# Kernel optimization log

Measured on AMD Instinct MI355X. Metric: run time of the kernel, lower is better.

Reference implementation:

```python
import jax, jax.numpy as jnp
import numpy as np
import math

B_SZ, L_SEQ, IN_DIM, D_MODEL, OUT_DIM = 8, 4096, 256, 512, 256
RMIN, RMAX = 0.8, 0.99


def setup_inputs() -> dict:
    key = jax.random.key(0)
    ks = jax.random.split(key, 9)
    inputs = jax.random.normal(ks[0], (B_SZ, L_SEQ, IN_DIM), dtype=jnp.float32)
    # A-parameterization per LRUBlock.init_A
    u1 = jax.random.uniform(ks[1], (D_MODEL,), dtype=jnp.float32)
    u2 = jax.random.uniform(ks[2], (D_MODEL,), dtype=jnp.float32)
    nu_log = jnp.log(-0.5 * jnp.log(u1 * (RMAX + RMIN) * (RMAX - RMIN) + RMIN ** 2))
    theta_log = jnp.log(2 * math.pi * u2)
    # NB: original stores gamma (not log gamma) and exponentiates it in forward; replicate.
    gamma_log = jnp.sqrt(1.0 - jnp.exp(-jnp.exp(nu_log)) ** 2)
    B_re = jax.random.uniform(ks[3], (D_MODEL, IN_DIM), dtype=jnp.float32) / math.sqrt(2 * IN_DIM)
    B_im = jax.random.uniform(ks[4], (D_MODEL, IN_DIM), dtype=jnp.float32) / math.sqrt(2 * IN_DIM)
    C_re = jax.random.uniform(ks[5], (OUT_DIM, D_MODEL), dtype=jnp.float32) / math.sqrt(D_MODEL)
    C_im = jax.random.uniform(ks[6], (OUT_DIM, D_MODEL), dtype=jnp.float32) / math.sqrt(D_MODEL)
    D = jax.random.uniform(ks[7], (OUT_DIM, IN_DIM), dtype=jnp.float32) / math.sqrt(IN_DIM)
    return {"inputs": inputs, "nu_log": nu_log, "theta_log": theta_log,
            "gamma_log": gamma_log, "B_re": B_re, "B_im": B_im,
            "C_re": C_re, "C_im": C_im, "D": D}


def reference(inputs, nu_log, theta_log, gamma_log, B_re, B_im, C_re, C_im, D):
    # skip connection: [b, l, in] x [out, in] -> [b, l, out]
    skip = jnp.einsum('blh,dh->bld', inputs, D)
    L = inputs.shape[1]
    # diagonal complex transition A = exp(-exp(nu) + i*exp(theta)), [d_model]
    A = jnp.exp(jax.lax.complex(-jnp.exp(nu_log), jnp.exp(theta_log)))
    Bc = jax.lax.complex(B_re, B_im) * jnp.exp(gamma_log)[:, None]
    # input projection u = inputs @ B^T : [b, l, d_model] complex64
    u = jnp.einsum('blh,dh->bld', inputs.astype(jnp.complex64), Bc)
    # convolution kernel H[d, t] = A[d]^t, linear conv via length-2L FFT
    H = A[:, None] ** jnp.arange(L)  # [d_model, L]
    n = 2 * L
    h_f = jnp.fft.fft(H, n=n, axis=1)          # [d_model, 2L]
    u_f = jnp.fft.fft(u, n=n, axis=1)          # [b, 2L, d_model]
    x = jnp.fft.ifft(u_f * h_f.T, axis=1)[:, :L]  # [b, L, d_model] complex64
    y = jnp.einsum('blh,nh->bln', x, jax.lax.complex(C_re, C_im)).real + skip
    return (x, y)
```

## Files before the change

kernel.cpp:

```cpp
#include <hip/hip_runtime.h>
#include <hip/hip_bf16.h>
#include <math.h>

#define B_SZ 8
#define L_SEQ 4096
#define IN_DIM 256
#define D_MODEL 512
#define OUT_DIM 256
#define M_ROWS (B_SZ*L_SEQ)
#define CH 64
#define NCH (L_SEQ/CH)

#define Y_OFF ((size_t)M_ROWS*D_MODEL)

#define XIM_B   ((size_t)0)
#define INPB_B  ((size_t)33554432)
#define WT_B    ((size_t)50331648)
#define CDT_B   ((size_t)50855936)
#define S_B     ((size_t)51511296)

typedef __attribute__((ext_vector_type(8))) short short8;
typedef __attribute__((ext_vector_type(4))) float f32x4;
typedef unsigned short ushort_t;
typedef unsigned int u32;

__device__ __forceinline__ unsigned short f2b(float f) {
    unsigned u = __float_as_uint(f);
    unsigned r = u + 0x7FFF + ((u >> 16) & 1);
    return (unsigned short)(r >> 16);
}
__device__ __forceinline__ float b2f(unsigned v) {
    return __uint_as_float(v << 16);
}
__device__ __forceinline__ unsigned pk2(float lo, float hi) {
    __hip_bfloat162 h = __float22bfloat162_rn(make_float2(lo, hi));
    return *(unsigned*)&h;
}
__device__ __forceinline__ void async16(const void* g, void* l) {
    __builtin_amdgcn_global_load_lds((const __attribute__((address_space(1))) u32*)g,
                                     (__attribute__((address_space(3))) u32*)l, 16, 0, 0);
}

__global__ __launch_bounds__(256) void cvt_inp(const float* __restrict__ inp, ushort_t* __restrict__ inpb) {
    size_t i = ((size_t)blockIdx.x*256 + threadIdx.x)*8;
    float4 a = *(const float4*)(inp + i);
    float4 b = *(const float4*)(inp + i + 4);
    unsigned v[4] = { pk2(a.x,a.y), pk2(a.z,a.w), pk2(b.x,b.y), pk2(b.z,b.w) };
    *(uint4*)(inpb + i) = *(uint4*)v;
}

__global__ void build_wt(const float* __restrict__ B_re, const float* __restrict__ B_im,
                         const float* __restrict__ gamma_log, ushort_t* __restrict__ Wt) {
    int idx = blockIdx.x*256 + threadIdx.x;
    int r = idx >> 8, h = idx & 255;
    int d = r >> 1, comp = r & 1;
    float eg = expf(gamma_log[d]);
    float v = (comp ? B_im[d*256 + h] : B_re[d*256 + h]) * eg;
    Wt[idx] = f2b(v);
}

__global__ void build_cdt(const float* __restrict__ C_re, const float* __restrict__ C_im,
                          const float* __restrict__ Dm, ushort_t* __restrict__ CDt) {
    int idx = blockIdx.x*256 + threadIdx.x;
    int n = idx / 1280, k = idx % 1280;
    float v;
    if      (k < 512)  v =  C_re[n*512 + k];
    else if (k < 1024) v = -C_im[n*512 + (k-512)];
    else               v =  Dm[n*256 + (k-1024)];
    CDt[idx] = f2b(v);
}

__global__ __launch_bounds__(256) void gemm_u(const ushort_t* __restrict__ inpb, const ushort_t* __restrict__ Wt,
                                              ushort_t* __restrict__ xpair) {
    __shared__ ushort_t Al[128*64];
    __shared__ ushort_t Bl[128*64];
    const int tid = threadIdx.x;
    int orig = blockIdx.x;
    int wg = (orig & 7) * 256 + (orig >> 3);
    const int row0 = (wg >> 3) * 128, col0 = (wg & 7) * 128;
    const int wave = tid >> 6, lane = tid & 63;
    const int wr = wave >> 1, wc = wave & 1;
    const int fr = lane & 15, kg = lane >> 4;
    const int grow = tid >> 3, ggr = tid & 7;
    f32x4 acc[4][4] = {};
    for (int k0 = 0; k0 < IN_DIM; k0 += 64) {
        __syncthreads();
        #pragma unroll
        for (int i = 0; i < 4; ++i) {
            int row = grow + i*32;
            async16(inpb + (size_t)(row0+row)*IN_DIM + k0 + ggr*8, &Al[(row*8 + ggr)*8]);
        }
        #pragma unroll
        for (int i = 0; i < 4; ++i) {
            int row = grow + i*32;
            async16(Wt + (size_t)(col0+row)*IN_DIM + k0 + ggr*8, &Bl[(row*8 + ggr)*8]);
        }
        __syncthreads();
        #pragma unroll
        for (int kk = 0; kk < 2; ++kk) {
            short8 af[4], bf[4];
            #pragma unroll
            for (int m = 0; m < 4; ++m) af[m] = *(const short8*)&Al[(wr*64 + m*16 + fr)*64 + kk*32 + kg*8];
            #pragma unroll
            for (int n = 0; n < 4; ++n) bf[n] = *(const short8*)&Bl[(wc*64 + n*16 + fr)*64 + kk*32 + kg*8];
            #pragma unroll
            for (int m = 0; m < 4; ++m)
                #pragma unroll
                for (int n = 0; n < 4; ++n)
                    acc[m][n] = __builtin_amdgcn_mfma_f32_16x16x32_bf16(af[m], bf[n], acc[m][n], 0, 0, 0);
        }
    }
    #pragma unroll
    for (int m = 0; m < 4; ++m)
        #pragma unroll
        for (int n = 0; n < 4; ++n) {
            int col = col0 + wc*64 + n*16 + fr;
            #pragma unroll
            for (int j = 0; j < 4; ++j) {
                int row = row0 + wr*64 + m*16 + kg*4 + j;
                xpair[(size_t)row*1024 + col] = f2b(acc[m][n][j]);
            }
        }
}

__global__ __launch_bounds__(256) void gemm_y(const float* __restrict__ xre, const ushort_t* __restrict__ xim,
                                              const ushort_t* __restrict__ inpb, const ushort_t* __restrict__ CDt,
                                              float* __restrict__ y) {
    __shared__ ushort_t Al[128*64];
    __shared__ ushort_t Bl[128*64];
    const int tid = threadIdx.x;
    int orig = blockIdx.x;
    int wg = (orig & 7) * 64 + (orig >> 3);
    const int row0 = (wg >> 1) * 128, col0 = (wg & 1) * 128;
    const int wave = tid >> 6, lane = tid & 63;
    const int wr = wave >> 1, wc = wave & 1;
    const int fr = lane & 15, kg = lane >> 4;
    const int grow = tid >> 3, ggr = tid & 7;
    const int crow = tid >> 1, csh = (tid & 1)*32;
    f32x4 acc[4][4] = {};
    for (int ks = 0; ks < 20; ++ks) {
        const int k0 = ks*64;
        __syncthreads();
        if (ks < 8) {
            const float* ap = xre + (size_t)(row0+crow)*D_MODEL + k0 + csh;
            unsigned v[16];
            #pragma unroll
            for (int i = 0; i < 8; ++i) {
                float4 f = *(const float4*)(ap + i*4);
                v[2*i]   = pk2(f.x, f.y);
                v[2*i+1] = pk2(f.z, f.w);
            }
            #pragma unroll
            for (int i = 0; i < 4; ++i) {
                int row = grow + i*32;
                async16(CDt + (size_t)(col0+row)*1280 + k0 + ggr*8, &Bl[(row*8 + ggr)*8]);
            }
            ushort_t* dst = &Al[crow*64 + csh];
            #pragma unroll
            for (int i = 0; i < 4; ++i) *(uint4*)(dst + i*8) = *(uint4*)&v[i*4];
        } else {
            const ushort_t* asrc;
            size_t stride; int kc;
            if (ks < 16) { asrc = xim;  stride = D_MODEL; kc = k0 - 512; }
            else         { asrc = inpb; stride = IN_DIM;  kc = k0 - 1024; }
            #pragma unroll
            for (int i = 0; i < 4; ++i) {
                int row = grow + i*32;
                async16(asrc + (size_t)(row0+row)*stride + kc + ggr*8, &Al[(row*8 + ggr)*8]);
            }
            #pragma unroll
            for (int i = 0; i < 4; ++i) {
                int row = grow + i*32;
                async16(CDt + (size_t)(col0+row)*1280 + k0 + ggr*8, &Bl[(row*8 + ggr)*8]);
            }
        }
        __syncthreads();
        #pragma unroll
        for (int kk = 0; kk < 2; ++kk) {
            short8 af[4], bf[4];
            #pragma unroll
            for (int m = 0; m < 4; ++m) af[m] = *(const short8*)&Al[(wr*64 + m*16 + fr)*64 + kk*32 + kg*8];
            #pragma unroll
            for (int n = 0; n < 4; ++n) bf[n] = *(const short8*)&Bl[(wc*64 + n*16 + fr)*64 + kk*32 + kg*8];
            #pragma unroll
            for (int m = 0; m < 4; ++m)
                #pragma unroll
                for (int n = 0; n < 4; ++n)
                    acc[m][n] = __builtin_amdgcn_mfma_f32_16x16x32_bf16(af[m], bf[n], acc[m][n], 0, 0, 0);
        }
    }
    #pragma unroll
    for (int m = 0; m < 4; ++m)
        #pragma unroll
        for (int n = 0; n < 4; ++n) {
            int col = col0 + wc*64 + n*16 + fr;
            #pragma unroll
            for (int j = 0; j < 4; ++j) {
                int row = row0 + wr*64 + m*16 + kg*4 + j;
                y[(size_t)row*OUT_DIM + col] = acc[m][n][j];
            }
        }
}

__global__ void scan_phase1(const unsigned* __restrict__ xp,
                            const float* __restrict__ nu_log, const float* __restrict__ theta_log,
                            float2* __restrict__ s) {
    int idx = blockIdx.x*256 + threadIdx.x;
    int d = idx & (D_MODEL-1);
    int c = (idx >> 9) & (NCH-1);
    int b = idx >> 15;
    float en = expf(nu_log[d]), et = expf(theta_log[d]);
    float mag = expf(-en);
    float ar = mag*cosf(et), ai = mag*sinf(et);
    float hr = 0.f, hi = 0.f;
    size_t off = ((size_t)(b*L_SEQ) + c*CH)*D_MODEL + d;
    #pragma unroll 4
    for (int j = 0; j < CH; ++j) {
        unsigned p = xp[off];
        float ur = b2f(p & 0xffffu), ui = b2f(p >> 16);
        float nr = ar*hr - ai*hi + ur;
        float ni = ar*hi + ai*hr + ui;
        hr = nr; hi = ni;
        off += D_MODEL;
    }
    s[idx] = make_float2(hr, hi);
}

__global__ void scan_phase2(const float* __restrict__ nu_log, const float* __restrict__ theta_log,
                            float2* __restrict__ s) {
    int idx = blockIdx.x*256 + threadIdx.x;
    int d = idx & (D_MODEL-1);
    int b = idx >> 9;
    float en = expf(nu_log[d]), et = expf(theta_log[d]);
    float mag = expf(-(float)CH*en);
    float ang = (float)CH*et;
    float aCr = mag*cosf(ang), aCi = mag*sinf(ang);
    float er = 0.f, ei = 0.f;
    float2* sp = s + (size_t)b*NCH*D_MODEL + d;
    for (int c8 = 0; c8 < NCH; c8 += 8) {
        float2 v[8];
        #pragma unroll
        for (int i = 0; i < 8; ++i) v[i] = sp[(size_t)(c8+i)*D_MODEL];
        #pragma unroll
        for (int i = 0; i < 8; ++i) {
            sp[(size_t)(c8+i)*D_MODEL] = make_float2(er, ei);
            float nr = aCr*er - aCi*ei + v[i].x;
            float ni = aCr*ei + aCi*er + v[i].y;
            er = nr; ei = ni;
        }
    }
}

__global__ void scan_phase3(unsigned* __restrict__ xp, ushort_t* __restrict__ xim,
                            const float* __restrict__ nu_log, const float* __restrict__ theta_log,
                            const float2* __restrict__ s) {
    int idx = blockIdx.x*256 + threadIdx.x;
    int d = idx & (D_MODEL-1);
    int c = (idx >> 9) & (NCH-1);
    int b = idx >> 15;
    float en = expf(nu_log[d]), et = expf(theta_log[d]);
    float mag = expf(-en);
    float ar = mag*cosf(et), ai = mag*sinf(et);
    float2 carry = s[idx];
    float hr = carry.x, hi = carry.y;
    size_t off = ((size_t)(b*L_SEQ) + c*CH)*D_MODEL + d;
    #pragma unroll 4
    for (int j = 0; j < CH; ++j) {
        unsigned p = xp[off];
        float ur = b2f(p & 0xffffu), ui = b2f(p >> 16);
        float nr = ar*hr - ai*hi + ur;
        float ni = ar*hi + ai*hr + ui;
        hr = nr; hi = ni;
        xp[off] = __float_as_uint(hr);
        xim[off] = f2b(hi);
        off += D_MODEL;
    }
}

extern "C" void kernel_launch(void* const* d_in, const int* in_sizes, int n_in,
                              void* d_out, int out_size, void* d_ws, size_t ws_size,
                              hipStream_t stream) {
    const float* inp       = (const float*)d_in[0];
    const float* nu_log    = (const float*)d_in[1];
    const float* theta_log = (const float*)d_in[2];
    const float* gamma_log = (const float*)d_in[3];
    const float* B_re      = (const float*)d_in[4];
    const float* B_im      = (const float*)d_in[5];
    const float* C_re      = (const float*)d_in[6];
    const float* C_im      = (const float*)d_in[7];
    const float* Dm        = (const float*)d_in[8];
    float* out = (float*)d_out;
    char* wsb  = (char*)d_ws;
    ushort_t* Xim  = (ushort_t*)(wsb + XIM_B);
    ushort_t* Inpb = (ushort_t*)(wsb + INPB_B);
    ushort_t* Wt   = (ushort_t*)(wsb + WT_B);
    ushort_t* CDt  = (ushort_t*)(wsb + CDT_B);
    float2*   S    = (float2*)  (wsb + S_B);

    build_wt<<<1024, 256, 0, stream>>>(B_re, B_im, gamma_log, Wt);
    build_cdt<<<1280, 256, 0, stream>>>(C_re, C_im, Dm, CDt);
    cvt_inp<<<(M_ROWS*IN_DIM)/(256*8), 256, 0, stream>>>(inp, Inpb);

    gemm_u<<<2048, 256, 0, stream>>>(Inpb, Wt, (ushort_t*)out);

    scan_phase1<<<(B_SZ*NCH*D_MODEL)/256, 256, 0, stream>>>((const unsigned*)out, nu_log, theta_log, S);
    scan_phase2<<<(B_SZ*D_MODEL)/256, 256, 0, stream>>>(nu_log, theta_log, S);
    scan_phase3<<<(B_SZ*NCH*D_MODEL)/256, 256, 0, stream>>>((unsigned*)out, Xim, nu_log, theta_log, S);

    gemm_y<<<512, 256, 0, stream>>>(out, Xim, Inpb, CDt, out + Y_OFF);
}
```

Baseline: 251.3 us.

## Keep scanned state as interleaved bf16 pairs in workspace and stage gemm_u stores via LDS

The u projection is now written to a workspace buffer instead of the output buffer. The scan writes interleaved bf16 (re,im) pairs back in place and writes the fp32 real part directly to the output. gemm_y then loads one contiguous bf16 A operand with async copies instead of converting fp32 real data on the fly, and CDt is reordered to match the interleaved K layout. gemm_u's epilogue goes through a swizzled LDS tile so global stores are coalesced 16-byte writes. This needs a larger workspace, and the imaginary part is still rounded to bf16 before the output GEMM as before.

```diff
diff --git a/kernel.cpp b/kernel.cpp
--- a/kernel.cpp
+++ b/kernel.cpp
@@ -13,11 +13,11 @@
 
 #define Y_OFF ((size_t)M_ROWS*D_MODEL)
 
-#define XIM_B   ((size_t)0)
-#define INPB_B  ((size_t)33554432)
-#define WT_B    ((size_t)50331648)
-#define CDT_B   ((size_t)50855936)
-#define S_B     ((size_t)51511296)
+#define XP_B    ((size_t)0)
+#define INPB_B  ((size_t)67108864)
+#define WT_B    ((size_t)83886080)
+#define CDT_B   ((size_t)84410368)
+#define S_B     ((size_t)85065728)
 
 typedef __attribute__((ext_vector_type(8))) short short8;
 typedef __attribute__((ext_vector_type(4))) float f32x4;
@@ -64,16 +64,20 @@
     int idx = blockIdx.x*256 + threadIdx.x;
     int n = idx / 1280, k = idx % 1280;
     float v;
-    if      (k < 512)  v =  C_re[n*512 + k];
-    else if (k < 1024) v = -C_im[n*512 + (k-512)];
-    else               v =  Dm[n*256 + (k-1024)];
+    if (k < 1024) {
+        int d = k >> 1;
+        v = (k & 1) ? -C_im[n*512 + d] : C_re[n*512 + d];
+    } else {
+        v = Dm[n*256 + (k-1024)];
+    }
     CDt[idx] = f2b(v);
 }
 
 __global__ __launch_bounds__(256) void gemm_u(const ushort_t* __restrict__ inpb, const ushort_t* __restrict__ Wt,
                                               ushort_t* __restrict__ xpair) {
-    __shared__ ushort_t Al[128*64];
-    __shared__ ushort_t Bl[128*64];
+    __shared__ ushort_t lds[128*128];
+    ushort_t* Al = lds;
+    ushort_t* Bl = lds + 128*64;
     const int tid = threadIdx.x;
     int orig = blockIdx.x;
     int wg = (orig & 7) * 256 + (orig >> 3);
@@ -110,24 +114,36 @@
                     acc[m][n] = __builtin_amdgcn_mfma_f32_16x16x32_bf16(af[m], bf[n], acc[m][n], 0, 0, 0);
         }
     }
+    __syncthreads();
     #pragma unroll
     for (int m = 0; m < 4; ++m)
         #pragma unroll
         for (int n = 0; n < 4; ++n) {
-            int col = col0 + wc*64 + n*16 + fr;
+            int colb = wc*64 + n*16 + fr;
             #pragma unroll
             for (int j = 0; j < 4; ++j) {
-                int row = row0 + wr*64 + m*16 + kg*4 + j;
-                xpair[(size_t)row*1024 + col] = f2b(acc[m][n][j]);
+                int row = wr*64 + m*16 + kg*4 + j;
+                int q = ((row >> 2) ^ row) & 3;
+                lds[row*128 + (colb ^ (q << 4))] = f2b(acc[m][n][j]);
             }
         }
-}
-
-__global__ __launch_bounds__(256) void gemm_y(const float* __restrict__ xre, const ushort_t* __restrict__ xim,
+    __syncthreads();
+    const int seg = tid & 15, rbase = tid >> 4;
+    #pragma unroll
+    for (int p = 0; p < 8; ++p) {
+        int row = rbase + p*16;
+        int q = ((row >> 2) ^ row) & 3;
+        uint4 v = *(const uint4*)&lds[row*128 + ((seg*8) ^ (q << 4))];
+        *(uint4*)&xpair[(size_t)(row0+row)*1024 + col0 + seg*8] = v;
+    }
+}
+
+__global__ __launch_bounds__(256) void gemm_y(const ushort_t* __restrict__ xp,
                                               const ushort_t* __restrict__ inpb, const ushort_t* __restrict__ CDt,
                                               float* __restrict__ y) {
-    __shared__ ushort_t Al[128*64];
-    __shared__ ushort_t Bl[128*64];
+    __shared__ ushort_t lds[128*128];
+    ushort_t* Al = lds;
+    ushort_t* Bl = lds + 128*64;
     const int tid = threadIdx.x;
     int orig = blockIdx.x;
     int wg = (orig & 7) * 64 + (orig >> 3);
@@ -136,43 +152,27 @@
     const int wr = wave >> 1, wc = wave & 1;
     const int fr = lane & 15, kg = lane >> 4;
     const int grow = tid >> 3, ggr = tid & 7;
-    const int crow = tid >> 1, csh = (tid & 1)*32;
     f32x4 acc[4][4] = {};
     for (int ks = 0; ks < 20; ++ks) {
         const int k0 = ks*64;
         __syncthreads();
-        if (ks < 8) {
-            const float* ap = xre + (size_t)(row0+crow)*D_MODEL + k0 + csh;
-            unsigned v[16];
-            #pragma unroll
-            for (int i = 0; i < 8; ++i) {
-                float4 f = *(const float4*)(ap + i*4);
-                v[2*i]   = pk2(f.x, f.y);
-                v[2*i+1] = pk2(f.z, f.w);
-            }
+        if (ks < 16) {
             #pragma unroll
             for (int i = 0; i < 4; ++i) {
                 int row = grow + i*32;
-                async16(CDt + (size_t)(col0+row)*1280 + k0 + ggr*8, &Bl[(row*8 + ggr)*8]);
+                async16(xp + (size_t)(row0+row)*1024 + k0 + ggr*8, &Al[(row*8 + ggr)*8]);
             }
-            ushort_t* dst = &Al[crow*64 + csh];
-            #pragma unroll
-            for (int i = 0; i < 4; ++i) *(uint4*)(dst + i*8) = *(uint4*)&v[i*4];
         } else {
-            const ushort_t* asrc;
-            size_t stride; int kc;
-            if (ks < 16) { asrc = xim;  stride = D_MODEL; kc = k0 - 512; }
-            else         { asrc = inpb; stride = IN_DIM;  kc = k0 - 1024; }
             #pragma unroll
             for (int i = 0; i < 4; ++i) {
                 int row = grow + i*32;
-                async16(asrc + (size_t)(row0+row)*stride + kc + ggr*8, &Al[(row*8 + ggr)*8]);
+                async16(inpb + (size_t)(row0+row)*IN_DIM + (k0-1024) + ggr*8, &Al[(row*8 + ggr)*8]);
             }
-            #pragma unroll
-            for (int i = 0; i < 4; ++i) {
-                int row = grow + i*32;
-                async16(CDt + (size_t)(col0+row)*1280 + k0 + ggr*8, &Bl[(row*8 + ggr)*8]);
-            }
+        }
+        #pragma unroll
+        for (int i = 0; i < 4; ++i) {
+            int row = grow + i*32;
+            async16(CDt + (size_t)(col0+row)*1280 + k0 + ggr*8, &Bl[(row*8 + ggr)*8]);
         }
         __syncthreads();
         #pragma unroll
@@ -251,7 +251,7 @@
     }
 }
 
-__global__ void scan_phase3(unsigned* __restrict__ xp, ushort_t* __restrict__ xim,
+__global__ void scan_phase3(unsigned* __restrict__ xp, float* __restrict__ xre_out,
                             const float* __restrict__ nu_log, const float* __restrict__ theta_log,
                             const float2* __restrict__ s) {
     int idx = blockIdx.x*256 + threadIdx.x;
@@ -271,8 +271,8 @@
         float nr = ar*hr - ai*hi + ur;
         float ni = ar*hi + ai*hr + ui;
         hr = nr; hi = ni;
-        xp[off] = __float_as_uint(hr);
-        xim[off] = f2b(hi);
+        xp[off] = pk2(hr, hi);
+        xre_out[off] = hr;
         off += D_MODEL;
     }
 }
@@ -291,7 +291,7 @@
     const float* Dm        = (const float*)d_in[8];
     float* out = (float*)d_out;
     char* wsb  = (char*)d_ws;
-    ushort_t* Xim  = (ushort_t*)(wsb + XIM_B);
+    ushort_t* XP   = (ushort_t*)(wsb + XP_B);
     ushort_t* Inpb = (ushort_t*)(wsb + INPB_B);
     ushort_t* Wt   = (ushort_t*)(wsb + WT_B);
     ushort_t* CDt  = (ushort_t*)(wsb + CDT_B);
@@ -301,11 +301,11 @@
     build_cdt<<<1280, 256, 0, stream>>>(C_re, C_im, Dm, CDt);
     cvt_inp<<<(M_ROWS*IN_DIM)/(256*8), 256, 0, stream>>>(inp, Inpb);
 
-    gemm_u<<<2048, 256, 0, stream>>>(Inpb, Wt, (ushort_t*)out);
-
-    scan_phase1<<<(B_SZ*NCH*D_MODEL)/256, 256, 0, stream>>>((const unsigned*)out, nu_log, theta_log, S);
+    gemm_u<<<2048, 256, 0, stream>>>(Inpb, Wt, XP);
+
+    scan_phase1<<<(B_SZ*NCH*D_MODEL)/256, 256, 0, stream>>>((const unsigned*)XP, nu_log, theta_log, S);
     scan_phase2<<<(B_SZ*D_MODEL)/256, 256, 0, stream>>>(nu_log, theta_log, S);
-    scan_phase3<<<(B_SZ*NCH*D_MODEL)/256, 256, 0, stream>>>((unsigned*)out, Xim, nu_log, theta_log, S);
-
-    gemm_y<<<512, 256, 0, stream>>>(out, Xim, Inpb, CDt, out + Y_OFF);
-}
+    scan_phase3<<<(B_SZ*NCH*D_MODEL)/256, 256, 0, stream>>>((unsigned*)XP, out, nu_log, theta_log, S);
+
+    gemm_y<<<512, 256, 0, stream>>>(XP, Inpb, CDt, out + Y_OFF);
+}
```

Measured after the change: 244.6 us. 1.03x faster.
